# Kernel tuning notes

Hardware: AMD Instinct MI355X
Metric: run time of the kernel (lower is better)

The kernel has to match this reference:

```python
import jax, jax.numpy as jnp
import numpy as np

D_MODEL = 1024
NUM_HEADS = 16
HEAD_DIM = D_MODEL // NUM_HEADS
ALPHA = 1.0


def setup_inputs() -> dict:
    key = jax.random.key(0)
    ks = jax.random.split(key, 9)
    B, T, D = 2, 2048, D_MODEL
    s = 1.0 / np.sqrt(D)
    inp = {
        "x": jax.random.normal(ks[0], (B, T, D), dtype=jnp.float32),
        "Wq": jax.random.uniform(ks[1], (D, D), jnp.float32, -s, s),
        "bq": jax.random.uniform(ks[2], (D,), jnp.float32, -s, s),
        "Wk": jax.random.uniform(ks[3], (D, D), jnp.float32, -s, s),
        "bk": jax.random.uniform(ks[4], (D,), jnp.float32, -s, s),
        "Wv": jax.random.uniform(ks[5], (D, D), jnp.float32, -s, s),
        "bv": jax.random.uniform(ks[6], (D,), jnp.float32, -s, s),
        "Wo": jax.random.uniform(ks[7], (D, D), jnp.float32, -s, s),
        "bo": jax.random.uniform(ks[8], (D,), jnp.float32, -s, s),
    }
    return inp


def reference(x, Wq, bq, Wk, bk, Wv, bv, Wo, bo):
    B, T, D = x.shape
    H, hd = NUM_HEADS, HEAD_DIM

    def split_heads(y):  # [B,T,D] -> [B,H,T,hd]
        return y.reshape(B, T, H, hd).transpose(0, 2, 1, 3)

    Q = split_heads(x @ Wq.T + bq)
    K = split_heads(x @ Wk.T + bk)
    V = split_heads(x @ Wv.T + bv)

    scores = jnp.einsum('bhid,bhjd->bhij', Q, K) / jnp.sqrt(jnp.float32(hd))

    t = jnp.arange(T)
    delta = t[:, None] - t[None, :]  # [T,T], i - j
    causal_mask = delta < 0          # j > i (strict upper triangle)
    # similarity_power_law decay bias: -(delta)^alpha for delta >= 0, else 0
    decay = jnp.where(causal_mask, 0.0, -(delta.astype(jnp.float32) ** ALPHA))

    scores = jnp.where(causal_mask, -jnp.inf, scores) + decay
    attn = jax.nn.softmax(scores, axis=-1)

    out = jnp.einsum('bhij,bhjd->bhid', attn, V)
    out = out.transpose(0, 2, 1, 3).reshape(B, T, D)
    return out @ Wo.T + bo
```

## Files before the change

kernel.cpp:

```cpp
#include <hip/hip_runtime.h>

#define TT 2048
#define DD 1024
#define HH 16
#define HD 64
#define NTOK 4096

typedef __bf16 bf16x8 __attribute__((ext_vector_type(8)));
typedef short short4v __attribute__((ext_vector_type(4)));
typedef float f32x4 __attribute__((ext_vector_type(4)));

__device__ __forceinline__ unsigned short f2bf(float f) {
  unsigned u = __float_as_uint(f);
  u += 0x7fffu + ((u >> 16) & 1u);
  return (unsigned short)(u >> 16);
}

#if __has_builtin(__builtin_amdgcn_mfma_f32_16x16x16bf16_1k)
__device__ __forceinline__ f32x4 mfma16(short4v a, short4v b, f32x4 c) {
  return __builtin_amdgcn_mfma_f32_16x16x16bf16_1k(a, b, c, 0, 0, 0);
}
#else
__device__ __forceinline__ f32x4 mfma16(short4v a, short4v b, f32x4 c) {
  asm("v_mfma_f32_16x16x16_bf16 %0, %1, %2, %0\n\ts_nop 7\n\ts_nop 7"
      : "+v"(c) : "v"(a), "v"(b));
  return c;
}
#endif

typedef void __attribute__((address_space(1))) as1_void;
typedef void __attribute__((address_space(3))) as3_void;
__device__ __forceinline__ void gl_lds16(const void* g, void* l) {
  __builtin_amdgcn_global_load_lds((as1_void*)g, (as3_void*)l, 16, 0, 0);
}

__global__ __launch_bounds__(256)
void wcmha_cast_all(const float4* __restrict__ x,  const float4* __restrict__ wq,
                    const float4* __restrict__ wk, const float4* __restrict__ wv,
                    const float4* __restrict__ wo,
                    ushort4* __restrict__ xb,  ushort4* __restrict__ wqb,
                    ushort4* __restrict__ wkb, ushort4* __restrict__ wvb,
                    ushort4* __restrict__ wob) {
  const int i = blockIdx.x * 256 + threadIdx.x;
  const float4* src;
  ushort4* dst;
  int off;
  if (i < 1048576) {
    src = x; dst = xb; off = i;
  } else {
    int j = i - 1048576;
    int sel = j >> 18;
    off = j & 262143;
    const float4* ws_[4] = {wq, wk, wv, wo};
    ushort4* wd_[4] = {wqb, wkb, wvb, wob};
    src = ws_[sel]; dst = wd_[sel];
  }
  float4 v = src[off];
  ushort4 o;
  o.x = f2bf(v.x); o.y = f2bf(v.y); o.z = f2bf(v.z); o.w = f2bf(v.w);
  dst[off] = o;
}

template <int BN_, bool SWAP>
__device__ __forceinline__ void gemm_db(const unsigned short* __restrict__ X,
                                        const unsigned short* __restrict__ W,
                                        int m0, int n0,
                                        unsigned short* As, unsigned short* Bs,
                                        f32x4 acc[4][BN_ / 32]) {
  constexpr int NI = BN_ / 32;
  constexpr int JB = (BN_ * 4) / 256;
  const int tid = threadIdx.x, wid = tid >> 6, lane = tid & 63;
  const int m = lane & 15, quad = lane >> 4;
  const int wm = (wid >> 1) * 64, wn = (wid & 1) * (BN_ / 2);
  const int xq = (quad ^ ((m >> 1) & 3)) * 8;

  const unsigned short* gA[2];
  const unsigned short* gB[JB];
#pragma unroll
  for (int j = 0; j < 2; ++j) {
    int c = wid * 64 + lane + j * 256;
    gA[j] = X + (size_t)(m0 + (c >> 2)) * DD + ((c & 3) ^ ((c >> 3) & 3)) * 8;
  }
#pragma unroll
  for (int j = 0; j < JB; ++j) {
    int c = wid * 64 + lane + j * 256;
    gB[j] = W + (size_t)(n0 + (c >> 2)) * DD + ((c & 3) ^ ((c >> 3) & 3)) * 8;
  }
  unsigned short* lA[2][2];
  unsigned short* lB[2][JB];
#pragma unroll
  for (int p = 0; p < 2; ++p) {
#pragma unroll
    for (int j = 0; j < 2; ++j)
      lA[p][j] = As + p * (128 * 32) + (wid * 64 + j * 256) * 8;
#pragma unroll
    for (int j = 0; j < JB; ++j)
      lB[p][j] = Bs + p * (BN_ * 32) + (wid * 64 + j * 256) * 8;
  }

#pragma unroll
  for (int i = 0; i < 4; ++i)
#pragma unroll
    for (int j = 0; j < NI; ++j) acc[i][j] = (f32x4){0.f, 0.f, 0.f, 0.f};

#pragma unroll
  for (int j = 0; j < 2; ++j) gl_lds16(gA[j], lA[0][j]);
#pragma unroll
  for (int j = 0; j < JB; ++j) gl_lds16(gB[j], lB[0][j]);

  for (int k = 0; k < 32; ++k) {
    const int p = k & 1;
    __syncthreads();
    if (k < 31) {
      const int k1 = (k + 1) * 32;
#pragma unroll
      for (int j = 0; j < 2; ++j) gl_lds16(gA[j] + k1, lA[p ^ 1][j]);
#pragma unroll
      for (int j = 0; j < JB; ++j) gl_lds16(gB[j] + k1, lB[p ^ 1][j]);
    }
    const unsigned short* ap = As + p * (128 * 32);
    const unsigned short* bp = Bs + p * (BN_ * 32);
    bf16x8 af[4], bf[NI];
#pragma unroll
    for (int mi = 0; mi < 4; ++mi)
      af[mi] = *(const bf16x8*)&ap[(wm + mi * 16 + m) * 32 + xq];
#pragma unroll
    for (int ni = 0; ni < NI; ++ni)
      bf[ni] = *(const bf16x8*)&bp[(wn + ni * 16 + m) * 32 + xq];
#pragma unroll
    for (int mi = 0; mi < 4; ++mi)
#pragma unroll
      for (int ni = 0; ni < NI; ++ni)
        acc[mi][ni] = SWAP
            ? __builtin_amdgcn_mfma_f32_16x16x32_bf16(bf[ni], af[mi], acc[mi][ni], 0, 0, 0)
            : __builtin_amdgcn_mfma_f32_16x16x32_bf16(af[mi], bf[ni], acc[mi][ni], 0, 0, 0);
  }
}

__global__ __launch_bounds__(256)
void wcmha_gemm_qkv(const unsigned short* __restrict__ X,
                    const unsigned short* __restrict__ Wq,
                    const unsigned short* __restrict__ Wk,
                    const unsigned short* __restrict__ Wv,
                    const float* __restrict__ bq, const float* __restrict__ bk,
                    const float* __restrict__ bv,
                    unsigned short* __restrict__ Qb,
                    unsigned short* __restrict__ Kb,
                    unsigned short* __restrict__ Vt) {
  __shared__ unsigned short As[2 * 128 * 32];
  __shared__ unsigned short Bs[2 * 128 * 32];
  const int mat = blockIdx.y >> 3;
  const int m0 = blockIdx.x * 128;
  const int n0 = (blockIdx.y & 7) * 128;

  const int lane = threadIdx.x & 63, wid = threadIdx.x >> 6;
  const int m = lane & 15, quad = lane >> 4;
  const int wm = (wid >> 1) * 64, wn = (wid & 1) * 64;

  f32x4 acc[4][4];
  if (mat < 2) {
    const unsigned short* W = mat ? Wk : Wq;
    const float* bias = mat ? bk : bq;
    unsigned short* dst = mat ? Kb : Qb;
    gemm_db<128, true>(X, W, m0, n0, As, Bs, acc);
#pragma unroll
    for (int mi = 0; mi < 4; ++mi) {
      int row = m0 + wm + mi * 16 + m;
      int b = row >> 11, t = row & (TT - 1);
#pragma unroll
      for (int ni = 0; ni < 4; ++ni) {
        int col0 = n0 + wn + ni * 16 + quad * 4;
        int h = col0 >> 6, d0 = col0 & 63;
        float4 bb = *(const float4*)&bias[col0];
        short4v v;
        v[0] = (short)f2bf(acc[mi][ni][0] + bb.x);
        v[1] = (short)f2bf(acc[mi][ni][1] + bb.y);
        v[2] = (short)f2bf(acc[mi][ni][2] + bb.z);
        v[3] = (short)f2bf(acc[mi][ni][3] + bb.w);
        *(short4v*)&dst[((size_t)(b * HH + h) * TT + t) * HD + d0] = v;
      }
    }
  } else {
    gemm_db<128, false>(X, Wv, m0, n0, As, Bs, acc);
#pragma unroll
    for (int ni = 0; ni < 4; ++ni) {
      int col = n0 + wn + ni * 16 + m;
      int h = col >> 6, d = col & 63;
      float bb = bv[col];
#pragma unroll
      for (int mi = 0; mi < 4; ++mi) {
        int row0 = m0 + wm + mi * 16 + quad * 4;
        int b = row0 >> 11, t0 = row0 & (TT - 1);
        short4v v;
#pragma unroll
        for (int r = 0; r < 4; ++r) v[r] = (short)f2bf(acc[mi][ni][r] + bb);
        *(short4v*)&Vt[((size_t)(b * HH + h) * HD + d) * TT + t0] = v;
      }
    }
  }
}

__global__ __launch_bounds__(256)
void wcmha_gemm_out(const unsigned short* __restrict__ X,
                    const unsigned short* __restrict__ W,
                    const float* __restrict__ bias,
                    float* __restrict__ Y) {
  __shared__ unsigned short As[2 * 128 * 32];
  __shared__ unsigned short Bs[2 * 64 * 32];
  const int m0 = blockIdx.x * 128;
  const int n0 = blockIdx.y * 64;
  const int lane = threadIdx.x & 63, wid = threadIdx.x >> 6;
  const int m = lane & 15, quad = lane >> 4;
  const int wm = (wid >> 1) * 64, wn = (wid & 1) * 32;

  f32x4 acc[4][2];
  gemm_db<64, true>(X, W, m0, n0, As, Bs, acc);

#pragma unroll
  for (int mi = 0; mi < 4; ++mi) {
    int row = m0 + wm + mi * 16 + m;
#pragma unroll
    for (int ni = 0; ni < 2; ++ni) {
      int col0 = n0 + wn + ni * 16 + quad * 4;
      float4 bb = *(const float4*)&bias[col0];
      float4 o;
      o.x = acc[mi][ni][0] + bb.x;
      o.y = acc[mi][ni][1] + bb.y;
      o.z = acc[mi][ni][2] + bb.z;
      o.w = acc[mi][ni][3] + bb.w;
      *(float4*)&Y[(size_t)row * DD + col0] = o;
    }
  }
}

__global__ __launch_bounds__(256)
void wcmha_attn(const unsigned short* __restrict__ Qb,
                const unsigned short* __restrict__ Kb,
                const unsigned short* __restrict__ Vt,
                unsigned short* __restrict__ O) {
  const int wid = threadIdx.x >> 6, lane = threadIdx.x & 63;
  const int gw = (blockIdx.x << 2) + wid;
  const int qt = gw & 127, bh = gw >> 7;
  const int qbase = qt << 4;
  const int il = lane & 15, quad = lane >> 4;
  const int ig = qbase + il;

  const unsigned short* q_ptr = Qb + (size_t)bh * TT * HD;
  const unsigned short* k_ptr = Kb + (size_t)bh * TT * HD;
  const unsigned short* v_ptr = Vt + (size_t)bh * HD * TT;

  const bf16x8 qf0 = *(const bf16x8*)(q_ptr + (size_t)ig * HD + quad * 8);
  const bf16x8 qf1 = *(const bf16x8*)(q_ptr + (size_t)ig * HD + 32 + quad * 8);

  const int j0 = (qbase >= 48) ? qbase - 48 : 0;

  f32x4 st[4];
#pragma unroll
  for (int jt = 0; jt < 4; ++jt) {
    const unsigned short* kp = k_ptr + (size_t)(j0 + jt * 16 + il) * HD;
    bf16x8 k0 = *(const bf16x8*)(kp + quad * 8);
    bf16x8 k1 = *(const bf16x8*)(kp + 32 + quad * 8);
    f32x4 a = {0.f, 0.f, 0.f, 0.f};
    a = __builtin_amdgcn_mfma_f32_16x16x32_bf16(k0, qf0, a, 0, 0, 0);
    a = __builtin_amdgcn_mfma_f32_16x16x32_bf16(k1, qf1, a, 0, 0, 0);
    st[jt] = a;
  }

  float mloc = -3.0e38f;
#pragma unroll
  for (int jt = 0; jt < 4; ++jt)
#pragma unroll
    for (int r = 0; r < 4; ++r) {
      int jg = j0 + jt * 16 + quad * 4 + r;
      float v = (jg > ig) ? -3.0e38f : st[jt][r] * 0.125f - (float)(ig - jg);
      st[jt][r] = v;
      mloc = fmaxf(mloc, v);
    }
  mloc = fmaxf(mloc, __shfl_xor(mloc, 16));
  mloc = fmaxf(mloc, __shfl_xor(mloc, 32));

  float rs = 0.f;
  short4v pf[4];
#pragma unroll
  for (int jt = 0; jt < 4; ++jt)
#pragma unroll
    for (int r = 0; r < 4; ++r) {
      float p = __expf(st[jt][r] - mloc);
      rs += p;
      pf[jt][r] = (short)f2bf(p);
    }
  rs += __shfl_xor(rs, 16);
  rs += __shfl_xor(rs, 32);

  f32x4 o_acc[4];
#pragma unroll
  for (int nt = 0; nt < 4; ++nt) o_acc[nt] = (f32x4){0.f, 0.f, 0.f, 0.f};
#pragma unroll
  for (int jt = 0; jt < 4; ++jt)
#pragma unroll
    for (int nt = 0; nt < 4; ++nt) {
      short4v vf = *(const short4v*)(v_ptr + (size_t)(nt * 16 + il) * TT +
                                     j0 + jt * 16 + quad * 4);
      o_acc[nt] = mfma16(vf, pf[jt], o_acc[nt]);
    }

  const float inv_l = 1.f / rs;
  const int b = bh >> 4, hh = bh & 15;
  unsigned short* ob = O + ((size_t)(b * TT + ig)) * DD + hh * HD;
#pragma unroll
  for (int nt = 0; nt < 4; ++nt)
#pragma unroll
    for (int r = 0; r < 4; ++r)
      ob[nt * 16 + quad * 4 + r] = f2bf(o_acc[nt][r] * inv_l);
}

extern "C" void kernel_launch(void* const* d_in, const int* in_sizes, int n_in,
                              void* d_out, int out_size, void* d_ws, size_t ws_size,
                              hipStream_t stream) {
  const float* x  = (const float*)d_in[0];
  const float* Wq = (const float*)d_in[1];
  const float* bq = (const float*)d_in[2];
  const float* Wk = (const float*)d_in[3];
  const float* bk = (const float*)d_in[4];
  const float* Wv = (const float*)d_in[5];
  const float* bv = (const float*)d_in[6];
  const float* Wo = (const float*)d_in[7];
  const float* bo = (const float*)d_in[8];

  char* ws = (char*)d_ws;
  unsigned short* xb  = (unsigned short*)(ws);
  unsigned short* wqb = (unsigned short*)(ws + (8u << 20));
  unsigned short* wkb = wqb + (1u << 20);
  unsigned short* wvb = wkb + (1u << 20);
  unsigned short* wob = wvb + (1u << 20);
  unsigned short* Qb  = (unsigned short*)(ws + (16u << 20));
  unsigned short* Kb  = (unsigned short*)(ws + (24u << 20));
  unsigned short* Vt  = (unsigned short*)(ws + (32u << 20));
  unsigned short* Ob  = xb;

  wcmha_cast_all<<<8192, 256, 0, stream>>>(
      (const float4*)x, (const float4*)Wq, (const float4*)Wk,
      (const float4*)Wv, (const float4*)Wo,
      (ushort4*)xb, (ushort4*)wqb, (ushort4*)wkb, (ushort4*)wvb, (ushort4*)wob);

  wcmha_gemm_qkv<<<dim3(32, 24), 256, 0, stream>>>(xb, wqb, wkb, wvb,
                                                   bq, bk, bv, Qb, Kb, Vt);

  wcmha_attn<<<1024, 256, 0, stream>>>(Qb, Kb, Vt, Ob);

  wcmha_gemm_out<<<dim3(32, 16), 256, 0, stream>>>(Ob, wob, bo, (float*)d_out);
}
```

Before: 163.3 us.

## Widen cast stores, unroll GEMM k-loop by two, vectorize attention output stores

The cast kernel now converts eight floats per thread and writes 16-byte vectors, using half as many blocks. The GEMM mainloop is manually unrolled by two with fixed buffer indices and uses 32-bit byte offsets instead of 64-bit pointers, cutting address arithmetic and branches. The attention epilogue packs four bf16 values into a single 8-byte store instead of four scalar stores. Together these reduce instruction overhead and memory transactions, at the cost of more code size and register use.

```diff
diff --git a/kernel.cpp b/kernel.cpp
--- a/kernel.cpp
+++ b/kernel.cpp
@@ -9,6 +9,7 @@
 typedef __bf16 bf16x8 __attribute__((ext_vector_type(8)));
 typedef short short4v __attribute__((ext_vector_type(4)));
 typedef float f32x4 __attribute__((ext_vector_type(4)));
+typedef unsigned short ushort8v __attribute__((ext_vector_type(8)));
 
 __device__ __forceinline__ unsigned short f2bf(float f) {
   unsigned u = __float_as_uint(f);
@@ -38,26 +39,28 @@
 void wcmha_cast_all(const float4* __restrict__ x,  const float4* __restrict__ wq,
                     const float4* __restrict__ wk, const float4* __restrict__ wv,
                     const float4* __restrict__ wo,
-                    ushort4* __restrict__ xb,  ushort4* __restrict__ wqb,
-                    ushort4* __restrict__ wkb, ushort4* __restrict__ wvb,
-                    ushort4* __restrict__ wob) {
+                    ushort8v* __restrict__ xb,  ushort8v* __restrict__ wqb,
+                    ushort8v* __restrict__ wkb, ushort8v* __restrict__ wvb,
+                    ushort8v* __restrict__ wob) {
   const int i = blockIdx.x * 256 + threadIdx.x;
   const float4* src;
-  ushort4* dst;
+  ushort8v* dst;
   int off;
-  if (i < 1048576) {
+  if (i < 524288) {
     src = x; dst = xb; off = i;
   } else {
-    int j = i - 1048576;
-    int sel = j >> 18;
-    off = j & 262143;
+    int j = i - 524288;
+    int sel = j >> 17;
+    off = j & 131071;
     const float4* ws_[4] = {wq, wk, wv, wo};
-    ushort4* wd_[4] = {wqb, wkb, wvb, wob};
+    ushort8v* wd_[4] = {wqb, wkb, wvb, wob};
     src = ws_[sel]; dst = wd_[sel];
   }
-  float4 v = src[off];
-  ushort4 o;
-  o.x = f2bf(v.x); o.y = f2bf(v.y); o.z = f2bf(v.z); o.w = f2bf(v.w);
+  float4 a = src[off * 2];
+  float4 b = src[off * 2 + 1];
+  ushort8v o;
+  o[0] = f2bf(a.x); o[1] = f2bf(a.y); o[2] = f2bf(a.z); o[3] = f2bf(a.w);
+  o[4] = f2bf(b.x); o[5] = f2bf(b.y); o[6] = f2bf(b.z); o[7] = f2bf(b.w);
   dst[off] = o;
 }
 
@@ -74,17 +77,16 @@
   const int wm = (wid >> 1) * 64, wn = (wid & 1) * (BN_ / 2);
   const int xq = (quad ^ ((m >> 1) & 3)) * 8;
 
-  const unsigned short* gA[2];
-  const unsigned short* gB[JB];
+  unsigned aoff[2], boff[JB];
 #pragma unroll
   for (int j = 0; j < 2; ++j) {
     int c = wid * 64 + lane + j * 256;
-    gA[j] = X + (size_t)(m0 + (c >> 2)) * DD + ((c & 3) ^ ((c >> 3) & 3)) * 8;
+    aoff[j] = (unsigned)(((m0 + (c >> 2)) * DD + ((c & 3) ^ ((c >> 3) & 3)) * 8) * 2);
   }
 #pragma unroll
   for (int j = 0; j < JB; ++j) {
     int c = wid * 64 + lane + j * 256;
-    gB[j] = W + (size_t)(n0 + (c >> 2)) * DD + ((c & 3) ^ ((c >> 3) & 3)) * 8;
+    boff[j] = (unsigned)(((n0 + (c >> 2)) * DD + ((c & 3) ^ ((c >> 3) & 3)) * 8) * 2);
   }
   unsigned short* lA[2][2];
   unsigned short* lB[2][JB];
@@ -103,38 +105,53 @@
 #pragma unroll
     for (int j = 0; j < NI; ++j) acc[i][j] = (f32x4){0.f, 0.f, 0.f, 0.f};
 
-#pragma unroll
-  for (int j = 0; j < 2; ++j) gl_lds16(gA[j], lA[0][j]);
-#pragma unroll
-  for (int j = 0; j < JB; ++j) gl_lds16(gB[j], lB[0][j]);
-
-  for (int k = 0; k < 32; ++k) {
-    const int p = k & 1;
+  const char* Xc = (const char*)X;
+  const char* Wc = (const char*)W;
+
+#define STAGE(kstep, p)                                                       \
+  {                                                                           \
+    const char* xk = Xc + (kstep) * 64;       \
+    const char* wk_ = Wc + (kstep) * 64;                                      \
+    _Pragma("unroll")                                                         \
+    for (int j = 0; j < 2; ++j) gl_lds16(xk + aoff[j], lA[p][j]);             \
+    _Pragma("unroll")                                                         \
+    for (int j = 0; j < JB; ++j) gl_lds16(wk_ + boff[j], lB[p][j]);           \
+  }
+
+#define COMPUTE(p)                                                            \
+  {                                                                           \
+    const unsigned short* ap = As + (p) * (128 * 32);                         \
+    const unsigned short* bp = Bs + (p) * (BN_ * 32);                         \
+    bf16x8 af[4], bf[NI];                                                     \
+    _Pragma("unroll")                                                         \
+    for (int mi = 0; mi < 4; ++mi)                                            \
+      af[mi] = *(const bf16x8*)&ap[(wm + mi * 16 + m) * 32 + xq];             \
+    _Pragma("unroll")                                                         \
+    for (int ni = 0; ni < NI; ++ni)                                           \
+      bf[ni] = *(const bf16x8*)&bp[(wn + ni * 16 + m) * 32 + xq];             \
+    _Pragma("unroll")                                                         \
+    for (int mi = 0; mi < 4; ++mi)                                            \
+      _Pragma("unroll")                                                       \
+      for (int ni = 0; ni < NI; ++ni)                                         \
+        acc[mi][ni] = SWAP                                                    \
+            ? __builtin_amdgcn_mfma_f32_16x16x32_bf16(bf[ni], af[mi],         \
+                                                      acc[mi][ni], 0, 0, 0)   \
+            : __builtin_amdgcn_mfma_f32_16x16x32_bf16(af[mi], bf[ni],         \
+                                                      acc[mi][ni], 0, 0, 0);  \
+  }
+
+  STAGE(0, 0);
+#pragma unroll 1
+  for (int kk = 0; kk < 32; kk += 2) {
     __syncthreads();
-    if (k < 31) {
-      const int k1 = (k + 1) * 32;
-#pragma unroll
-      for (int j = 0; j < 2; ++j) gl_lds16(gA[j] + k1, lA[p ^ 1][j]);
-#pragma unroll
-      for (int j = 0; j < JB; ++j) gl_lds16(gB[j] + k1, lB[p ^ 1][j]);
-    }
-    const unsigned short* ap = As + p * (128 * 32);
-    const unsigned short* bp = Bs + p * (BN_ * 32);
-    bf16x8 af[4], bf[NI];
-#pragma unroll
-    for (int mi = 0; mi < 4; ++mi)
-      af[mi] = *(const bf16x8*)&ap[(wm + mi * 16 + m) * 32 + xq];
-#pragma unroll
-    for (int ni = 0; ni < NI; ++ni)
-      bf[ni] = *(const bf16x8*)&bp[(wn + ni * 16 + m) * 32 + xq];
-#pragma unroll
-    for (int mi = 0; mi < 4; ++mi)
-#pragma unroll
-      for (int ni = 0; ni < NI; ++ni)
-        acc[mi][ni] = SWAP
-            ? __builtin_amdgcn_mfma_f32_16x16x32_bf16(bf[ni], af[mi], acc[mi][ni], 0, 0, 0)
-            : __builtin_amdgcn_mfma_f32_16x16x32_bf16(af[mi], bf[ni], acc[mi][ni], 0, 0, 0);
-  }
+    STAGE(kk + 1, 1);
+    COMPUTE(0);
+    __syncthreads();
+    if (kk + 2 < 32) STAGE(kk + 2, 0);
+    COMPUTE(1);
+  }
+#undef STAGE
+#undef COMPUTE
 }
 
 __global__ __launch_bounds__(256)
@@ -308,10 +325,12 @@
   const int b = bh >> 4, hh = bh & 15;
   unsigned short* ob = O + ((size_t)(b * TT + ig)) * DD + hh * HD;
 #pragma unroll
-  for (int nt = 0; nt < 4; ++nt)
-#pragma unroll
-    for (int r = 0; r < 4; ++r)
-      ob[nt * 16 + quad * 4 + r] = f2bf(o_acc[nt][r] * inv_l);
+  for (int nt = 0; nt < 4; ++nt) {
+    short4v v;
+#pragma unroll
+    for (int r = 0; r < 4; ++r) v[r] = (short)f2bf(o_acc[nt][r] * inv_l);
+    *(short4v*)&ob[nt * 16 + quad * 4] = v;
+  }
 }
 
 extern "C" void kernel_launch(void* const* d_in, const int* in_sizes, int n_in,
@@ -338,10 +357,11 @@
   unsigned short* Vt  = (unsigned short*)(ws + (32u << 20));
   unsigned short* Ob  = xb;
 
-  wcmha_cast_all<<<8192, 256, 0, stream>>>(
+  wcmha_cast_all<<<4096, 256, 0, stream>>>(
       (const float4*)x, (const float4*)Wq, (const float4*)Wk,
       (const float4*)Wv, (const float4*)Wo,
-      (ushort4*)xb, (ushort4*)wqb, (ushort4*)wkb, (ushort4*)wvb, (ushort4*)wob);
+      (ushort8v*)xb, (ushort8v*)wqb, (ushort8v*)wkb, (ushort8v*)wvb,
+      (ushort8v*)wob);
 
   wcmha_gemm_qkv<<<dim3(32, 24), 256, 0, stream>>>(xb, wqb, wkb, wvb,
                                                    bq, bk, bv, Qb, Kb, Vt);
```

New measurement: 173.9 us. +6.5%, slower.
